# Optimization experiments

Hardware: AMD Instinct MI355X
Metric: run time of the kernel (lower is better)

The kernel has to match this reference:

```python
import jax, jax.numpy as jnp
import numpy as np

N_HEAD = 16
N_KV = 4
Q_PER_KV = N_HEAD // N_KV  # 4
HEAD_DIM = 64
SCALE = HEAD_DIM ** -0.5


def setup_inputs() -> dict:
    key = jax.random.key(0)
    k1, k2, k3, k4 = jax.random.split(key, 4)
    B, L, H = 2, 2048, 1024
    x = jax.random.normal(k1, (B, L, H), dtype=jnp.float32)
    Wq = jax.random.normal(k2, (H, H), dtype=jnp.float32) * 0.02
    Wkv = jax.random.normal(k3, (2 * H // Q_PER_KV, H), dtype=jnp.float32) * 0.02
    Wo = jax.random.normal(k4, (H, H), dtype=jnp.float32) * 0.02
    return {"x": x, "Wq": Wq, "Wkv": Wkv, "Wo": Wo}


def reference(x, Wq, Wkv, Wo):
    B, L, H = x.shape
    # projections (nn.Linear: y = x @ W.T)
    q = (x @ Wq.T).reshape(B, L, N_KV, Q_PER_KV, HEAD_DIM)
    kv = (x @ Wkv.T).reshape(B, L, N_KV, 2, HEAD_DIM)
    k = kv[:, :, :, 0, :]  # [B, L, N_KV, D]
    v = kv[:, :, :, 1, :]  # [B, L, N_KV, D]
    # scores: [B, n_kv, q_per_kv, L, L]
    qk = SCALE * jnp.einsum('blgpd,bmgd->bgplm', q, k)
    qk = qk.reshape(B, N_HEAD, L, L)
    # ALiBi: slope_h * tril(j - i)
    slopes = 2.0 ** (-8.0 / N_HEAD * (jnp.arange(N_HEAD, dtype=jnp.float32) + 1.0))
    pos = jnp.arange(L)
    rel = jnp.tril(pos[None, :] - pos[:, None]).astype(qk.dtype)  # [L, L]
    qk = qk + slopes[:, None, None] * rel[None]
    # causal mask
    causal = pos[None, :] <= pos[:, None]  # [L, L] lower-triangular True
    qk = jnp.where(causal[None, None], qk, -jnp.inf)
    score = jax.nn.softmax(qk, axis=-1).reshape(B, N_KV, Q_PER_KV, L, L)
    # attend values: [B, n_kv, q_per_kv, L, D]
    out = jnp.einsum('bgplm,bmgd->bgpld', score, v)
    out = out.reshape(B, N_HEAD, L, HEAD_DIM).transpose(0, 2, 1, 3).reshape(B, L, H)
    return out @ Wo.T
```

## Files before the change

### kernel.cpp

```cpp
#include <hip/hip_runtime.h>

typedef unsigned short u16;
typedef unsigned int u32;
typedef float f32x4 __attribute__((ext_vector_type(4)));
typedef float f32x16 __attribute__((ext_vector_type(16)));
typedef __bf16 bf16x8 __attribute__((ext_vector_type(8)));
typedef u32 u32x4 __attribute__((ext_vector_type(4)));

__device__ __forceinline__ u16 f2bf(float f) {
  u32 u = __builtin_bit_cast(u32, f);
  u32 r = (u + 0x7fffu + ((u >> 16) & 1u)) >> 16;
  return (u16)r;
}

__device__ __forceinline__ u32 pk2bf(float lo, float hi_) {
  u32 r;
  asm("v_cvt_pk_bf16_f32 %0, %1, %2" : "=v"(r) : "v"(lo), "v"(hi_));
  return r;
}

__device__ __forceinline__ void plswap(u32 &a, u32 &b) {
#if __has_builtin(__builtin_amdgcn_permlane32_swap)
  auto r = __builtin_amdgcn_permlane32_swap(a, b, false, false);
  a = r[0]; b = r[1];
#else
  asm volatile("v_permlane32_swap_b32 %0, %1" : "+v"(a), "+v"(b));
#endif
}

__device__ __forceinline__ float xhalf_max(float x) {
  u32 a = __builtin_bit_cast(u32, x), b = a;
  plswap(a, b);
  return fmaxf(__builtin_bit_cast(float, a), __builtin_bit_cast(float, b));
}
__device__ __forceinline__ float xhalf_sum(float x) {
  u32 a = __builtin_bit_cast(u32, x), b = a;
  plswap(a, b);
  return __builtin_bit_cast(float, a) + __builtin_bit_cast(float, b);
}

__device__ __forceinline__ void gll16(const u16* g, u16* l) {
  __builtin_amdgcn_global_load_lds(
      (const __attribute__((address_space(1))) void*)g,
      (__attribute__((address_space(3))) void*)l, 16, 0, 0);
}

__global__ __launch_bounds__(256) void cvt_kernel(
    const float4* __restrict__ x, const float4* __restrict__ wq,
    const float4* __restrict__ wkv, const float4* __restrict__ wo,
    uint2* __restrict__ xb, uint2* __restrict__ wqkvb, uint2* __restrict__ wob) {
  long i = (long)blockIdx.x * 256 + threadIdx.x;
  const float4* src; uint2* dst; long off;
  if (i < 1048576)      { src = x;   dst = xb;             off = i; }
  else if (i < 1310720) { src = wq;  dst = wqkvb;          off = i - 1048576; }
  else if (i < 1441792) { src = wkv; dst = wqkvb + 262144; off = i - 1310720; }
  else                  { src = wo;  dst = wob;            off = i - 1441792; }
  float4 v = src[off];
  uint2 o;
  o.x = ((u32)f2bf(v.y) << 16) | (u32)f2bf(v.x);
  o.y = ((u32)f2bf(v.w) << 16) | (u32)f2bf(v.z);
  dst[off] = o;
}

__device__ __forceinline__ void gemm_core(
    const u16* __restrict__ A, const u16* __restrict__ W, const int K,
    f32x4 acc[4][4], u16* As, u16* Ws) {
  const int t = threadIdx.x, lane = t & 63, w = t >> 6;
  const int wm = (w >> 1) * 64, wn = (w & 1) * 64;
  const long bm = (long)blockIdx.x * 128, bn = (long)blockIdx.y * 128;
  const int cc = lane & 15, kg8 = (lane >> 4) * 8;

  const int srow = w * 32 + (lane >> 2);
  const int scol = (lane & 3) * 8;
  const u16* Ag0 = &A[(bm + srow) * (long)K + scol];
  const u16* Ag1 = Ag0 + 16 * (long)K;
  const u16* Wg0 = &W[(bn + srow) * (long)K + scol];
  const u16* Wg1 = Wg0 + 16 * (long)K;
  u16* Al0 = As + (w * 32) * 32;
  u16* Al1 = Al0 + 16 * 32;
  u16* Wl0 = Ws + (w * 32) * 32;
  u16* Wl1 = Wl0 + 16 * 32;

#pragma unroll
  for (int i = 0; i < 4; i++)
#pragma unroll
    for (int j = 0; j < 4; j++) acc[i][j] = f32x4{0.f, 0.f, 0.f, 0.f};

  for (int k0 = 0; k0 < K; k0 += 32) {
    gll16(Ag0 + k0, Al0);
    gll16(Ag1 + k0, Al1);
    gll16(Wg0 + k0, Wl0);
    gll16(Wg1 + k0, Wl1);
    __syncthreads();
    bf16x8 af[4], wf[4];
#pragma unroll
    for (int i = 0; i < 4; i++) af[i] = *(const bf16x8*)&As[(wm + i * 16 + cc) * 32 + kg8];
#pragma unroll
    for (int j = 0; j < 4; j++) wf[j] = *(const bf16x8*)&Ws[(wn + j * 16 + cc) * 32 + kg8];
#pragma unroll
    for (int i = 0; i < 4; i++)
#pragma unroll
      for (int j = 0; j < 4; j++)
        acc[i][j] = __builtin_amdgcn_mfma_f32_16x16x32_bf16(af[i], wf[j], acc[i][j], 0, 0, 0);
    __syncthreads();
  }
}

__global__ __launch_bounds__(256) void gemm_qkv_kernel(
    const u16* __restrict__ A, const u16* __restrict__ W,
    u16* __restrict__ Qb, u16* __restrict__ Kb, u16* __restrict__ VTb) {
  __shared__ __align__(16) u16 As[128 * 32];
  __shared__ __align__(16) u16 Ws[128 * 32];
  f32x4 acc[4][4];
  gemm_core(A, W, 1024, acc, As, Ws);
  const int t = threadIdx.x, lane = t & 63, w = t >> 6;
  const int wm = (w >> 1) * 64, wn = (w & 1) * 64;
  const int bm = blockIdx.x * 128, bn = blockIdx.y * 128;
  const int rr = (lane >> 4) * 4, cc = lane & 15;
#pragma unroll
  for (int i = 0; i < 4; i++)
#pragma unroll
    for (int jf = 0; jf < 4; jf++)
#pragma unroll
      for (int j = 0; j < 4; j++) {
        int m = bm + wm + i * 16 + rr + j;
        int n = bn + wn + jf * 16 + cc;
        float v = acc[i][jf][j];
        if (n < 1024) {
          Qb[(long)m * 1024 + n] = f2bf(v * 0.18033688011112043f);
        } else {
          int c = n - 1024, g = c >> 7, rm = c & 127;
          int b = m >> 11, pos = m & 2047;
          long base = (long)(b * 4 + g);
          if (rm < 64) Kb[(base * 2048 + pos) * 64 + rm] = f2bf(v);
          else         VTb[(base * 64 + (rm - 64)) * 2048 + pos] = f2bf(v);
        }
      }
}

__global__ __launch_bounds__(256) void gemm_out_kernel(
    const u16* __restrict__ A, const u16* __restrict__ W, float* __restrict__ out) {
  __shared__ __align__(16) u16 As[128 * 32];
  __shared__ __align__(16) u16 Ws[128 * 32];
  f32x4 acc[4][4];
  gemm_core(A, W, 1024, acc, As, Ws);
  const int t = threadIdx.x, lane = t & 63, w = t >> 6;
  const int wm = (w >> 1) * 64, wn = (w & 1) * 64;
  const int bm = blockIdx.x * 128, bn = blockIdx.y * 128;
  const int rr = (lane >> 4) * 4, cc = lane & 15;
#pragma unroll
  for (int i = 0; i < 4; i++)
#pragma unroll
    for (int jf = 0; jf < 4; jf++)
#pragma unroll
      for (int j = 0; j < 4; j++) {
        int m = bm + wm + i * 16 + rr + j;
        int n = bn + wn + jf * 16 + cc;
        out[(long)m * 1024 + n] = acc[i][jf][j];
      }
}

__global__ __launch_bounds__(256, 4) void attn_kernel(
    const u16* __restrict__ Q, const u16* __restrict__ Kb,
    const u16* __restrict__ VTb, u16* __restrict__ AT) {
  __shared__ __align__(16) float Ol[4][32][36];
  __shared__ float ml[4][2][32];

  const int t = threadIdx.x, lane = t & 63, w = t >> 6;
  const int qt = 63 - (int)blockIdx.x;
  const int h = blockIdx.y, b = blockIdx.z;
  const int g = h >> 2;
  const int lam = lane & 31, hi = lane >> 5;
  const int qrow0 = qt * 32;
  const int kblocks = (qrow0 + 95) >> 6;

  const u16* Qrow = Q + ((long)(b * 2048 + qrow0 + lam)) * 1024 + h * 64 + hi * 8;
  bf16x8 qf0 = *(const bf16x8*)(Qrow);
  bf16x8 qf1 = *(const bf16x8*)(Qrow + 16);
  bf16x8 qf2 = *(const bf16x8*)(Qrow + 32);
  bf16x8 qf3 = *(const bf16x8*)(Qrow + 48);

  const u16* Kg = Kb  + ((long)(b * 4 + g)) * 2048 * 64;
  const u16* Vg = VTb + ((long)(b * 4 + g)) * 64 * 2048;

  f32x16 zv;
#pragma unroll
  for (int i = 0; i < 16; i++) zv[i] = 0.f;
  f32x16 acc0 = zv, acc1 = zv;
  float m = -1e30f, lsum = 0.f;

  const float slope2 = exp2f(-0.5f * (float)(h + 1)) * 1.44269504f;
  const float fqr = (float)(qrow0 + lam);

  auto qk_tile = [&](int koff) -> f32x16 {
    const u16* Ka = Kg + (long)(koff + lam) * 64 + hi * 8;
    bf16x8 k0 = *(const bf16x8*)(Ka);
    bf16x8 k1 = *(const bf16x8*)(Ka + 16);
    bf16x8 k2 = *(const bf16x8*)(Ka + 32);
    bf16x8 k3 = *(const bf16x8*)(Ka + 48);
    f32x16 s = zv;
    s = __builtin_amdgcn_mfma_f32_32x32x16_bf16(k0, qf0, s, 0, 0, 0);
    s = __builtin_amdgcn_mfma_f32_32x32x16_bf16(k1, qf1, s, 0, 0, 0);
    s = __builtin_amdgcn_mfma_f32_32x32x16_bf16(k2, qf2, s, 0, 0, 0);
    s = __builtin_amdgcn_mfma_f32_32x32x16_bf16(k3, qf3, s, 0, 0, 0);
    float kb0 = (float)(koff + 4 * hi) - fqr;
    if (koff + 31 > qrow0) {
#pragma unroll
      for (int r = 0; r < 16; r++) {
        float d = kb0 + (float)((r & 3) + 8 * (r >> 2));
        s[r] = (d > 0.f) ? -1e30f : s[r] + slope2 * d;
      }
    } else {
#pragma unroll
      for (int r = 0; r < 16; r++)
        s[r] += slope2 * (kb0 + (float)((r & 3) + 8 * (r >> 2)));
    }
    return s;
  };

  auto pv_tile = [&](const f32x16 &p, int koff) {
    u32 wd[8];
#pragma unroll
    for (int i = 0; i < 8; i++) wd[i] = pk2bf(p[2 * i], p[2 * i + 1]);
    plswap(wd[0], wd[2]); plswap(wd[1], wd[3]);
    plswap(wd[4], wd[6]); plswap(wd[5], wd[7]);
    bf16x8 pf0 = __builtin_bit_cast(bf16x8, u32x4{wd[0], wd[1], wd[2], wd[3]});
    bf16x8 pf1 = __builtin_bit_cast(bf16x8, u32x4{wd[4], wd[5], wd[6], wd[7]});
    const u16* Va = Vg + (long)lam * 2048 + koff + hi * 8;
    bf16x8 v00 = *(const bf16x8*)(Va);
    bf16x8 v01 = *(const bf16x8*)(Va + 16);
    bf16x8 v10 = *(const bf16x8*)(Va + 32 * 2048);
    bf16x8 v11 = *(const bf16x8*)(Va + 32 * 2048 + 16);
    acc0 = __builtin_amdgcn_mfma_f32_32x32x16_bf16(v00, pf0, acc0, 0, 0, 0);
    acc0 = __builtin_amdgcn_mfma_f32_32x32x16_bf16(v01, pf1, acc0, 0, 0, 0);
    acc1 = __builtin_amdgcn_mfma_f32_32x32x16_bf16(v10, pf0, acc1, 0, 0, 0);
    acc1 = __builtin_amdgcn_mfma_f32_32x32x16_bf16(v11, pf1, acc1, 0, 0, 0);
  };

  const int jb0 = (kblocks > w) ? (w + (((kblocks - 1 - w) >> 2) << 2)) : -1;
  for (int jb = jb0; jb >= 0; jb -= 4) {
    const int kbase = jb * 64;
    f32x16 st0 = qk_tile(kbase);
    f32x16 st1;
    const bool t1v = (kbase + 32 <= qrow0 + 31);
    if (t1v) {
      st1 = qk_tile(kbase + 32);
    } else {
#pragma unroll
      for (int r = 0; r < 16; r++) st1[r] = -1e30f;
    }

    float red[8];
#pragma unroll
    for (int i = 0; i < 8; i++)
      red[i] = fmaxf(fmaxf(st0[i], st0[i + 8]), fmaxf(st1[i], st1[i + 8]));
#pragma unroll
    for (int i = 0; i < 4; i++) red[i] = fmaxf(red[i], red[i + 4]);
    float pm = fmaxf(fmaxf(red[0], red[1]), fmaxf(red[2], red[3]));
    pm = xhalf_max(pm);
    if (!__all(pm <= m + 8.f)) {
      float mnew = fmaxf(m, pm);
      float al = exp2f(m - mnew);
      m = mnew;
      lsum *= al;
      acc0 *= al;
      acc1 *= al;
    }
#pragma unroll
    for (int r = 0; r < 16; r++) st0[r] = exp2f(st0[r] - m);
#pragma unroll
    for (int r = 0; r < 16; r++) st1[r] = exp2f(st1[r] - m);
    {
      float sr[8];
#pragma unroll
      for (int i = 0; i < 8; i++) sr[i] = (st0[i] + st0[i + 8]) + (st1[i] + st1[i + 8]);
#pragma unroll
      for (int i = 0; i < 4; i++) sr[i] += sr[i + 4];
      float rs = (sr[0] + sr[1]) + (sr[2] + sr[3]);
      lsum += xhalf_sum(rs);
    }

    pv_tile(st0, kbase);
    if (t1v) pv_tile(st1, kbase + 32);
  }

#pragma unroll
  for (int rq = 0; rq < 4; rq++)
    *(f32x4*)&Ol[w][lam][8 * rq + 4 * hi] =
        f32x4{acc0[4 * rq], acc0[4 * rq + 1], acc0[4 * rq + 2], acc0[4 * rq + 3]};
  if (hi == 0) { ml[w][0][lam] = m; ml[w][1][lam] = lsum; }
  __syncthreads();

  const int r = t >> 3, c0 = (t & 7) * 4;
  float M = fmaxf(fmaxf(ml[0][0][r], ml[1][0][r]), fmaxf(ml[2][0][r], ml[3][0][r]));
  float sc[4];
  float L = 0.f;
#pragma unroll
  for (int ww = 0; ww < 4; ww++) {
    sc[ww] = exp2f(ml[ww][0][r] - M);
    L += sc[ww] * ml[ww][1][r];
  }
  const float inv = 1.f / L;
  {
    float o[4] = {0.f, 0.f, 0.f, 0.f};
#pragma unroll
    for (int ww = 0; ww < 4; ww++)
#pragma unroll
      for (int i = 0; i < 4; i++) o[i] += sc[ww] * Ol[ww][r][c0 + i];
    uint2 ov;
    ov.x = ((u32)f2bf(o[1] * inv) << 16) | f2bf(o[0] * inv);
    ov.y = ((u32)f2bf(o[3] * inv) << 16) | f2bf(o[2] * inv);
    *(uint2*)&AT[((long)(b * 2048 + qrow0 + r)) * 1024 + h * 64 + c0] = ov;
  }
  __syncthreads();
#pragma unroll
  for (int rq = 0; rq < 4; rq++)
    *(f32x4*)&Ol[w][lam][8 * rq + 4 * hi] =
        f32x4{acc1[4 * rq], acc1[4 * rq + 1], acc1[4 * rq + 2], acc1[4 * rq + 3]};
  __syncthreads();
  {
    float o[4] = {0.f, 0.f, 0.f, 0.f};
#pragma unroll
    for (int ww = 0; ww < 4; ww++)
#pragma unroll
      for (int i = 0; i < 4; i++) o[i] += sc[ww] * Ol[ww][r][c0 + i];
    uint2 ov;
    ov.x = ((u32)f2bf(o[1] * inv) << 16) | f2bf(o[0] * inv);
    ov.y = ((u32)f2bf(o[3] * inv) << 16) | f2bf(o[2] * inv);
    *(uint2*)&AT[((long)(b * 2048 + qrow0 + r)) * 1024 + h * 64 + 32 + c0] = ov;
  }
}

extern "C" void kernel_launch(void* const* d_in, const int* in_sizes, int n_in,
                              void* d_out, int out_size, void* d_ws, size_t ws_size,
                              hipStream_t stream) {
  const float* x   = (const float*)d_in[0];
  const float* Wq  = (const float*)d_in[1];
  const float* Wkv = (const float*)d_in[2];
  const float* Wo  = (const float*)d_in[3];
  float* out = (float*)d_out;
  char* ws = (char*)d_ws;

  u16* xb    = (u16*)(ws);
  u16* wqkvb = (u16*)(ws + 8388608);
  u16* wob   = (u16*)(ws + 11534336);
  u16* Qb    = (u16*)(ws + 13631488);
  u16* Kb    = (u16*)(ws + 22020096);
  u16* VTb   = (u16*)(ws + 24117248);
  u16* AT    = (u16*)(ws + 26214400);

  cvt_kernel<<<6656, 256, 0, stream>>>(
      (const float4*)x, (const float4*)Wq, (const float4*)Wkv, (const float4*)Wo,
      (uint2*)xb, (uint2*)wqkvb, (uint2*)wob);

  gemm_qkv_kernel<<<dim3(32, 12), 256, 0, stream>>>(xb, wqkvb, Qb, Kb, VTb);

  attn_kernel<<<dim3(64, 16, 2), 256, 0, stream>>>(Qb, Kb, VTb, AT);

  gemm_out_kernel<<<dim3(32, 8), 256, 0, stream>>>(AT, wob, out);
}
```

Before: 232.6 us.

## Double-buffer GEMM LDS tiles and restructure attention inner loop with peeled masked tile

```diff
diff --git a/kernel.cpp b/kernel.cpp
--- a/kernel.cpp
+++ b/kernel.cpp
@@ -76,27 +76,35 @@
   const u16* Ag1 = Ag0 + 16 * (long)K;
   const u16* Wg0 = &W[(bn + srow) * (long)K + scol];
   const u16* Wg1 = Wg0 + 16 * (long)K;
-  u16* Al0 = As + (w * 32) * 32;
-  u16* Al1 = Al0 + 16 * 32;
-  u16* Wl0 = Ws + (w * 32) * 32;
-  u16* Wl1 = Wl0 + 16 * 32;
+  const int lbase = w * 32 * 32;
 
 #pragma unroll
   for (int i = 0; i < 4; i++)
 #pragma unroll
     for (int j = 0; j < 4; j++) acc[i][j] = f32x4{0.f, 0.f, 0.f, 0.f};
 
-  for (int k0 = 0; k0 < K; k0 += 32) {
-    gll16(Ag0 + k0, Al0);
-    gll16(Ag1 + k0, Al1);
-    gll16(Wg0 + k0, Wl0);
-    gll16(Wg1 + k0, Wl1);
-    __syncthreads();
+  gll16(Ag0, As + lbase);
+  gll16(Ag1, As + lbase + 512);
+  gll16(Wg0, Ws + lbase);
+  gll16(Wg1, Ws + lbase + 512);
+  __syncthreads();
+
+  const int nt = K / 32;
+  for (int ti = 0; ti < nt; ti++) {
+    const int cur = (ti & 1) * 4096;
+    const int nxt = cur ^ 4096;
+    if (ti + 1 < nt) {
+      const int k0 = (ti + 1) * 32;
+      gll16(Ag0 + k0, As + nxt + lbase);
+      gll16(Ag1 + k0, As + nxt + lbase + 512);
+      gll16(Wg0 + k0, Ws + nxt + lbase);
+      gll16(Wg1 + k0, Ws + nxt + lbase + 512);
+    }
     bf16x8 af[4], wf[4];
 #pragma unroll
-    for (int i = 0; i < 4; i++) af[i] = *(const bf16x8*)&As[(wm + i * 16 + cc) * 32 + kg8];
-#pragma unroll
-    for (int j = 0; j < 4; j++) wf[j] = *(const bf16x8*)&Ws[(wn + j * 16 + cc) * 32 + kg8];
+    for (int i = 0; i < 4; i++) af[i] = *(const bf16x8*)&As[cur + (wm + i * 16 + cc) * 32 + kg8];
+#pragma unroll
+    for (int j = 0; j < 4; j++) wf[j] = *(const bf16x8*)&Ws[cur + (wn + j * 16 + cc) * 32 + kg8];
 #pragma unroll
     for (int i = 0; i < 4; i++)
 #pragma unroll
@@ -109,8 +117,8 @@
 __global__ __launch_bounds__(256) void gemm_qkv_kernel(
     const u16* __restrict__ A, const u16* __restrict__ W,
     u16* __restrict__ Qb, u16* __restrict__ Kb, u16* __restrict__ VTb) {
-  __shared__ __align__(16) u16 As[128 * 32];
-  __shared__ __align__(16) u16 Ws[128 * 32];
+  __shared__ __align__(16) u16 As[8192];
+  __shared__ __align__(16) u16 Ws[8192];
   f32x4 acc[4][4];
   gemm_core(A, W, 1024, acc, As, Ws);
   const int t = threadIdx.x, lane = t & 63, w = t >> 6;
@@ -140,8 +148,8 @@
 
 __global__ __launch_bounds__(256) void gemm_out_kernel(
     const u16* __restrict__ A, const u16* __restrict__ W, float* __restrict__ out) {
-  __shared__ __align__(16) u16 As[128 * 32];
-  __shared__ __align__(16) u16 Ws[128 * 32];
+  __shared__ __align__(16) u16 As[8192];
+  __shared__ __align__(16) u16 Ws[8192];
   f32x4 acc[4][4];
   gemm_core(A, W, 1024, acc, As, Ws);
   const int t = threadIdx.x, lane = t & 63, w = t >> 6;
@@ -173,6 +181,7 @@
   const int lam = lane & 31, hi = lane >> 5;
   const int qrow0 = qt * 32;
   const int kblocks = (qrow0 + 95) >> 6;
+  const int jb_max = kblocks - 1;
 
   const u16* Qrow = Q + ((long)(b * 2048 + qrow0 + lam)) * 1024 + h * 64 + hi * 8;
   bf16x8 qf0 = *(const bf16x8*)(Qrow);
@@ -187,102 +196,130 @@
 #pragma unroll
   for (int i = 0; i < 16; i++) zv[i] = 0.f;
   f32x16 acc0 = zv, acc1 = zv;
-  float m = -1e30f, lsum = 0.f;
 
   const float slope2 = exp2f(-0.5f * (float)(h + 1)) * 1.44269504f;
-  const float fqr = (float)(qrow0 + lam);
-
-  auto qk_tile = [&](int koff) -> f32x16 {
-    const u16* Ka = Kg + (long)(koff + lam) * 64 + hi * 8;
+  float m = slope2 * (float)(qrow0 + lam);
+  float lsum = 0.f;
+
+  auto tile = [&](int kbase, bool masked) {
+    const u16* Ka = Kg + (long)(kbase + lam) * 64 + hi * 8;
     bf16x8 k0 = *(const bf16x8*)(Ka);
     bf16x8 k1 = *(const bf16x8*)(Ka + 16);
     bf16x8 k2 = *(const bf16x8*)(Ka + 32);
     bf16x8 k3 = *(const bf16x8*)(Ka + 48);
-    f32x16 s = zv;
-    s = __builtin_amdgcn_mfma_f32_32x32x16_bf16(k0, qf0, s, 0, 0, 0);
-    s = __builtin_amdgcn_mfma_f32_32x32x16_bf16(k1, qf1, s, 0, 0, 0);
-    s = __builtin_amdgcn_mfma_f32_32x32x16_bf16(k2, qf2, s, 0, 0, 0);
-    s = __builtin_amdgcn_mfma_f32_32x32x16_bf16(k3, qf3, s, 0, 0, 0);
-    float kb0 = (float)(koff + 4 * hi) - fqr;
-    if (koff + 31 > qrow0) {
+    f32x16 s0 = zv;
+    s0 = __builtin_amdgcn_mfma_f32_32x32x16_bf16(k0, qf0, s0, 0, 0, 0);
+    s0 = __builtin_amdgcn_mfma_f32_32x32x16_bf16(k1, qf1, s0, 0, 0, 0);
+    s0 = __builtin_amdgcn_mfma_f32_32x32x16_bf16(k2, qf2, s0, 0, 0, 0);
+    s0 = __builtin_amdgcn_mfma_f32_32x32x16_bf16(k3, qf3, s0, 0, 0, 0);
+    const bool t1v = !masked || (kbase + 32 <= qrow0 + 31);
+    f32x16 s1;
+    if (t1v) {
+      const u16* Kc = Ka + 32 * 64;
+      bf16x8 c0 = *(const bf16x8*)(Kc);
+      bf16x8 c1 = *(const bf16x8*)(Kc + 16);
+      bf16x8 c2 = *(const bf16x8*)(Kc + 32);
+      bf16x8 c3 = *(const bf16x8*)(Kc + 48);
+      s1 = zv;
+      s1 = __builtin_amdgcn_mfma_f32_32x32x16_bf16(c0, qf0, s1, 0, 0, 0);
+      s1 = __builtin_amdgcn_mfma_f32_32x32x16_bf16(c1, qf1, s1, 0, 0, 0);
+      s1 = __builtin_amdgcn_mfma_f32_32x32x16_bf16(c2, qf2, s1, 0, 0, 0);
+      s1 = __builtin_amdgcn_mfma_f32_32x32x16_bf16(c3, qf3, s1, 0, 0, 0);
+    } else {
+#pragma unroll
+      for (int r = 0; r < 16; r++) s1[r] = -1e30f;
+    }
+
+    const u16* Va = Vg + (long)lam * 2048 + kbase + hi * 8;
+    bf16x8 vA0 = *(const bf16x8*)(Va);
+    bf16x8 vA1 = *(const bf16x8*)(Va + 16);
+    bf16x8 vA2 = *(const bf16x8*)(Va + 32);
+    bf16x8 vA3 = *(const bf16x8*)(Va + 48);
+    bf16x8 vB0 = *(const bf16x8*)(Va + 65536);
+    bf16x8 vB1 = *(const bf16x8*)(Va + 65536 + 16);
+    bf16x8 vB2 = *(const bf16x8*)(Va + 65536 + 32);
+    bf16x8 vB3 = *(const bf16x8*)(Va + 65536 + 48);
+
+    const float ks0 = slope2 * (float)(kbase + 4 * hi);
+    const float ks1 = ks0 + slope2 * 32.f;
+    if (masked) {
+      const float db0 = (float)(kbase + 4 * hi - qrow0 - lam);
 #pragma unroll
       for (int r = 0; r < 16; r++) {
-        float d = kb0 + (float)((r & 3) + 8 * (r >> 2));
-        s[r] = (d > 0.f) ? -1e30f : s[r] + slope2 * d;
+        const float rbf = (float)((r & 3) + 8 * (r >> 2));
+        const float d0 = db0 + rbf;
+        s0[r] = (d0 > 0.f) ? -1e30f : s0[r] + (ks0 + slope2 * rbf);
+        s1[r] = (d0 + 32.f > 0.f) ? -1e30f : s1[r] + (ks1 + slope2 * rbf);
       }
     } else {
 #pragma unroll
-      for (int r = 0; r < 16; r++)
-        s[r] += slope2 * (kb0 + (float)((r & 3) + 8 * (r >> 2)));
-    }
-    return s;
-  };
-
-  auto pv_tile = [&](const f32x16 &p, int koff) {
-    u32 wd[8];
-#pragma unroll
-    for (int i = 0; i < 8; i++) wd[i] = pk2bf(p[2 * i], p[2 * i + 1]);
-    plswap(wd[0], wd[2]); plswap(wd[1], wd[3]);
-    plswap(wd[4], wd[6]); plswap(wd[5], wd[7]);
-    bf16x8 pf0 = __builtin_bit_cast(bf16x8, u32x4{wd[0], wd[1], wd[2], wd[3]});
-    bf16x8 pf1 = __builtin_bit_cast(bf16x8, u32x4{wd[4], wd[5], wd[6], wd[7]});
-    const u16* Va = Vg + (long)lam * 2048 + koff + hi * 8;
-    bf16x8 v00 = *(const bf16x8*)(Va);
-    bf16x8 v01 = *(const bf16x8*)(Va + 16);
-    bf16x8 v10 = *(const bf16x8*)(Va + 32 * 2048);
-    bf16x8 v11 = *(const bf16x8*)(Va + 32 * 2048 + 16);
-    acc0 = __builtin_amdgcn_mfma_f32_32x32x16_bf16(v00, pf0, acc0, 0, 0, 0);
-    acc0 = __builtin_amdgcn_mfma_f32_32x32x16_bf16(v01, pf1, acc0, 0, 0, 0);
-    acc1 = __builtin_amdgcn_mfma_f32_32x32x16_bf16(v10, pf0, acc1, 0, 0, 0);
-    acc1 = __builtin_amdgcn_mfma_f32_32x32x16_bf16(v11, pf1, acc1, 0, 0, 0);
-  };
-
-  const int jb0 = (kblocks > w) ? (w + (((kblocks - 1 - w) >> 2) << 2)) : -1;
-  for (int jb = jb0; jb >= 0; jb -= 4) {
-    const int kbase = jb * 64;
-    f32x16 st0 = qk_tile(kbase);
-    f32x16 st1;
-    const bool t1v = (kbase + 32 <= qrow0 + 31);
-    if (t1v) {
-      st1 = qk_tile(kbase + 32);
-    } else {
-#pragma unroll
-      for (int r = 0; r < 16; r++) st1[r] = -1e30f;
+      for (int r = 0; r < 16; r++) {
+        const float rbf = (float)((r & 3) + 8 * (r >> 2));
+        s0[r] += ks0 + slope2 * rbf;
+        s1[r] += ks1 + slope2 * rbf;
+      }
     }
 
     float red[8];
 #pragma unroll
     for (int i = 0; i < 8; i++)
-      red[i] = fmaxf(fmaxf(st0[i], st0[i + 8]), fmaxf(st1[i], st1[i + 8]));
+      red[i] = fmaxf(fmaxf(s0[i], s0[i + 8]), fmaxf(s1[i], s1[i + 8]));
 #pragma unroll
     for (int i = 0; i < 4; i++) red[i] = fmaxf(red[i], red[i + 4]);
     float pm = fmaxf(fmaxf(red[0], red[1]), fmaxf(red[2], red[3]));
     pm = xhalf_max(pm);
     if (!__all(pm <= m + 8.f)) {
-      float mnew = fmaxf(m, pm);
-      float al = exp2f(m - mnew);
+      const float mnew = fmaxf(m, pm);
+      const float al = exp2f(m - mnew);
       m = mnew;
       lsum *= al;
       acc0 *= al;
       acc1 *= al;
     }
 #pragma unroll
-    for (int r = 0; r < 16; r++) st0[r] = exp2f(st0[r] - m);
-#pragma unroll
-    for (int r = 0; r < 16; r++) st1[r] = exp2f(st1[r] - m);
+    for (int r = 0; r < 16; r++) s0[r] = exp2f(s0[r] - m);
+#pragma unroll
+    for (int r = 0; r < 16; r++) s1[r] = exp2f(s1[r] - m);
     {
       float sr[8];
 #pragma unroll
-      for (int i = 0; i < 8; i++) sr[i] = (st0[i] + st0[i + 8]) + (st1[i] + st1[i + 8]);
+      for (int i = 0; i < 8; i++) sr[i] = (s0[i] + s0[i + 8]) + (s1[i] + s1[i + 8]);
 #pragma unroll
       for (int i = 0; i < 4; i++) sr[i] += sr[i + 4];
-      float rs = (sr[0] + sr[1]) + (sr[2] + sr[3]);
-      lsum += xhalf_sum(rs);
-    }
-
-    pv_tile(st0, kbase);
-    if (t1v) pv_tile(st1, kbase + 32);
-  }
+      lsum += xhalf_sum((sr[0] + sr[1]) + (sr[2] + sr[3]));
+    }
+
+    {
+      u32 wd[8];
+#pragma unroll
+      for (int i = 0; i < 8; i++) wd[i] = pk2bf(s0[2 * i], s0[2 * i + 1]);
+      plswap(wd[0], wd[2]); plswap(wd[1], wd[3]);
+      plswap(wd[4], wd[6]); plswap(wd[5], wd[7]);
+      bf16x8 pf0 = __builtin_bit_cast(bf16x8, u32x4{wd[0], wd[1], wd[2], wd[3]});
+      bf16x8 pf1 = __builtin_bit_cast(bf16x8, u32x4{wd[4], wd[5], wd[6], wd[7]});
+      acc0 = __builtin_amdgcn_mfma_f32_32x32x16_bf16(vA0, pf0, acc0, 0, 0, 0);
+      acc0 = __builtin_amdgcn_mfma_f32_32x32x16_bf16(vA1, pf1, acc0, 0, 0, 0);
+      acc1 = __builtin_amdgcn_mfma_f32_32x32x16_bf16(vB0, pf0, acc1, 0, 0, 0);
+      acc1 = __builtin_amdgcn_mfma_f32_32x32x16_bf16(vB1, pf1, acc1, 0, 0, 0);
+    }
+    if (t1v) {
+      u32 wd[8];
+#pragma unroll
+      for (int i = 0; i < 8; i++) wd[i] = pk2bf(s1[2 * i], s1[2 * i + 1]);
+      plswap(wd[0], wd[2]); plswap(wd[1], wd[3]);
+      plswap(wd[4], wd[6]); plswap(wd[5], wd[7]);
+      bf16x8 pf0 = __builtin_bit_cast(bf16x8, u32x4{wd[0], wd[1], wd[2], wd[3]});
+      bf16x8 pf1 = __builtin_bit_cast(bf16x8, u32x4{wd[4], wd[5], wd[6], wd[7]});
+      acc0 = __builtin_amdgcn_mfma_f32_32x32x16_bf16(vA2, pf0, acc0, 0, 0, 0);
+      acc0 = __builtin_amdgcn_mfma_f32_32x32x16_bf16(vA3, pf1, acc0, 0, 0, 0);
+      acc1 = __builtin_amdgcn_mfma_f32_32x32x16_bf16(vB2, pf0, acc1, 0, 0, 0);
+      acc1 = __builtin_amdgcn_mfma_f32_32x32x16_bf16(vB3, pf1, acc1, 0, 0, 0);
+    }
+  };
+
+  int jb = (kblocks > w) ? (w + (((kblocks - 1 - w) >> 2) << 2)) : -1;
+  if (jb == jb_max && jb >= 0) { tile(jb * 64, true); jb -= 4; }
+  for (; jb >= 0; jb -= 4) tile(jb * 64, false);
 
 #pragma unroll
   for (int rq = 0; rq < 4; rq++)
```

Result: slower. 325.9 us (+40.1%).
